# Kernel optimization log

Hardware: AMD Instinct MI355X
Metric: run time of the kernel (lower is better)

Reference implementation:

```python
import jax, jax.numpy as jnp
import numpy as np

DIM = 1024
N_HEADS = 16
HEAD_DIM = DIM // N_HEADS
FREQS = [31.0, 37.0, 41.0, 43.0, 47.0]
TWO_PI = 2.0 * float(np.pi)


def setup_inputs() -> dict:
    key = jax.random.key(0)
    ks = jax.random.split(key, 16)
    B, L = 2, 1024
    s = 0.02
    inp = {
        'x': jax.random.normal(ks[0], (B, L, DIM), dtype=jnp.float32),
        'Wq': jax.random.normal(ks[1], (DIM, DIM), dtype=jnp.float32) * s,
        'bq': jnp.zeros((DIM,), dtype=jnp.float32),
        'Wk': jax.random.normal(ks[2], (DIM, DIM), dtype=jnp.float32) * s,
        'bk': jnp.zeros((DIM,), dtype=jnp.float32),
        'Wv': jax.random.normal(ks[3], (DIM, DIM), dtype=jnp.float32) * s,
        'bv': jnp.zeros((DIM,), dtype=jnp.float32),
        'Wo': jax.random.normal(ks[4], (DIM, DIM), dtype=jnp.float32) * s,
        'bo': jnp.zeros((DIM,), dtype=jnp.float32),
        'alpha': jax.random.normal(ks[5], (N_HEADS, len(FREQS)), dtype=jnp.float32) * 0.1,
        'phi': jax.random.uniform(ks[6], (N_HEADS, len(FREQS)), dtype=jnp.float32) * TWO_PI,
        'temperature': jnp.ones((1,), dtype=jnp.float32),
        'gamma': jnp.ones((DIM,), dtype=jnp.float32),
        'beta': jnp.zeros((DIM,), dtype=jnp.float32),
    }
    return inp


def reference(x, Wq, bq, Wk, bk, Wv, bv, Wo, bo, alpha, phi, temperature, gamma, beta):
    B, L, D = x.shape
    H, hd = N_HEADS, HEAD_DIM
    # projections (torch Linear: y = x @ W.T + b), split heads -> (B,H,L,hd)
    q = (x @ Wq.T + bq).reshape(B, L, H, hd).transpose(0, 2, 1, 3)
    k = (x @ Wk.T + bk).reshape(B, L, H, hd).transpose(0, 2, 1, 3)
    v = (x @ Wv.T + bv).reshape(B, L, H, hd).transpose(0, 2, 1, 3)
    # similarity (B,H,L,L)
    sim = jnp.einsum('bhid,bhjd->bhij', q, k) / jnp.sqrt(jnp.asarray(hd, x.dtype))
    temp = jnp.abs(temperature)[0] + 0.1
    sim = sim / temp
    # multi-frequency holographic scores: sum_f alpha_f * sin(2*pi*sim/p_f + phi_f)
    scores = jnp.zeros_like(sim)
    for fi, freq in enumerate(FREQS):
        a = alpha[:, fi][None, :, None, None]
        p = phi[:, fi][None, :, None, None]
        scores = scores + a * jnp.sin(TWO_PI * sim / freq + p)
    # sigmoid-sum normalization (not softmax)
    w = jax.nn.sigmoid(scores)
    w = w / (jnp.sum(w, axis=-1, keepdims=True) + 1e-10)
    out = jnp.einsum('bhij,bhjd->bhid', w, v)
    out = out.transpose(0, 2, 1, 3).reshape(B, L, D)
    out = out @ Wo.T + bo
    # LayerNorm (eps=1e-5, biased variance)
    mu = jnp.mean(out, axis=-1, keepdims=True)
    var = jnp.mean(jnp.square(out - mu), axis=-1, keepdims=True)
    return (out - mu) / jnp.sqrt(var + 1e-5) * gamma + beta
```

## Files before the change

kernel.cpp:

```cpp
#include <hip/hip_runtime.h>
#include <hip/hip_bf16.h>

typedef short bf16x8 __attribute__((ext_vector_type(8)));
typedef float f32x4 __attribute__((ext_vector_type(4)));

#define MFMA16(a, b, c) __builtin_amdgcn_mfma_f32_16x16x32_bf16(a, b, c, 0, 0, 0)

static constexpr int SEQ = 1024;
static constexpr int DIM = 1024;
static constexpr int NH = 16;
static constexpr int HD = 64;

#if __has_builtin(__builtin_amdgcn_rcpf)
#define FAST_RCP(x) __builtin_amdgcn_rcpf(x)
#else
#define FAST_RCP(x) (1.0f / (x))
#endif

#if __has_builtin(__builtin_amdgcn_exp2f)
#define EXP2F(x) __builtin_amdgcn_exp2f(x)
#else
#define EXP2F(x) exp2f(x)
#endif

__device__ __forceinline__ int swz(int r) { return r ^ (r >> 3); }

__device__ __forceinline__ void gload16(const __hip_bfloat16* g, __hip_bfloat16* l)
{
    typedef const __attribute__((address_space(1))) unsigned GU;
    typedef __attribute__((address_space(3))) unsigned LU;
    __builtin_amdgcn_global_load_lds((GU*)g, (LU*)l, 16, 0, 0);
}

__global__ __launch_bounds__(256) void cvt_all(
    const float* __restrict__ x,  const float* __restrict__ wq,
    const float* __restrict__ wk, const float* __restrict__ wv,
    const float* __restrict__ wo,
    __hip_bfloat16* __restrict__ xb,  __hip_bfloat16* __restrict__ wqb,
    __hip_bfloat16* __restrict__ wkb, __hip_bfloat16* __restrict__ wvb,
    __hip_bfloat16* __restrict__ wob)
{
    const int reg = blockIdx.y;
    const float* src; __hip_bfloat16* dst; int n;
    if      (reg == 0) { src = x;  dst = xb;  n = 2 * SEQ * DIM; }
    else if (reg == 1) { src = wq; dst = wqb; n = DIM * DIM; }
    else if (reg == 2) { src = wk; dst = wkb; n = DIM * DIM; }
    else if (reg == 3) { src = wv; dst = wvb; n = DIM * DIM; }
    else               { src = wo; dst = wob; n = DIM * DIM; }
    const int i = (blockIdx.x * 256 + threadIdx.x) * 4;
    if (i < n) {
        float4 v = *(const float4*)(src + i);
        __hip_bfloat16 t[4];
        t[0] = __float2bfloat16(v.x); t[1] = __float2bfloat16(v.y);
        t[2] = __float2bfloat16(v.z); t[3] = __float2bfloat16(v.w);
        *(ushort4*)(dst + i) = *(ushort4*)t;
    }
}

__global__ __launch_bounds__(256) void gemm_qkv(
    const __hip_bfloat16* __restrict__ A,
    const __hip_bfloat16* __restrict__ W0, const __hip_bfloat16* __restrict__ W1,
    const __hip_bfloat16* __restrict__ W2,
    const float* __restrict__ b0, const float* __restrict__ b1,
    const float* __restrict__ b2,
    __hip_bfloat16* __restrict__ Y0, __hip_bfloat16* __restrict__ Y1,
    __hip_bfloat16* __restrict__ Y2,
    int M, int N, int K)
{
    __shared__ __align__(16) __hip_bfloat16 As[64 * 64];
    __shared__ __align__(16) __hip_bfloat16 Ws[128 * 64];

    const int z = blockIdx.z;
    const __hip_bfloat16* W = (z == 0) ? W0 : ((z == 1) ? W1 : W2);
    const float* bias = (z == 0) ? b0 : ((z == 1) ? b1 : b2);
    __hip_bfloat16* Y = (z == 0) ? Y0 : ((z == 1) ? Y1 : Y2);

    const int tid = threadIdx.x;
    const int wv = tid >> 6, lane = tid & 63;
    const int col16 = lane & 15, quad = lane >> 4;
    const int m0 = blockIdx.x * 64, n0 = blockIdx.y * 128;
    const int wr = wv >> 1, wc = wv & 1;

    const int scol = ((tid & 7) ^ ((tid >> 3) & 7)) * 8;
    const __hip_bfloat16* ga = A + (size_t)(m0 + (tid >> 3)) * K + scol;
    const __hip_bfloat16* gb = W + (size_t)(n0 + (tid >> 3)) * K + scol;
    __hip_bfloat16* lA = As + wv * 512;
    __hip_bfloat16* lB = Ws + wv * 512;

    const int c7 = col16 & 7;
    const int so0 = ((quad)     ^ c7) * 8;
    const int so1 = ((quad + 4) ^ c7) * 8;
    const __hip_bfloat16* ar = As + (wr * 32 + col16) * 64;
    const __hip_bfloat16* br = Ws + (wc * 64 + col16) * 64;

    f32x4 acc[8] = {};

    for (int k0 = 0; k0 < K; k0 += 64) {
        gload16(ga + k0,                  lA);
        gload16(ga + k0 + (size_t)32 * K, lA + 2048);
        gload16(gb + k0,                  lB);
        gload16(gb + k0 + (size_t)32 * K, lB + 2048);
        gload16(gb + k0 + (size_t)64 * K, lB + 4096);
        gload16(gb + k0 + (size_t)96 * K, lB + 6144);
        __syncthreads();
#pragma unroll
        for (int kh = 0; kh < 2; ++kh) {
            const int so = (kh == 0) ? so0 : so1;
            bf16x8 af[2], bfm[4];
#pragma unroll
            for (int mt = 0; mt < 2; ++mt) af[mt] = *(const bf16x8*)(ar + mt * 16 * 64 + so);
#pragma unroll
            for (int nt = 0; nt < 4; ++nt) bfm[nt] = *(const bf16x8*)(br + nt * 16 * 64 + so);
#pragma unroll
            for (int mt = 0; mt < 2; ++mt)
#pragma unroll
                for (int nt = 0; nt < 4; ++nt)
                    acc[mt * 4 + nt] = MFMA16(af[mt], bfm[nt], acc[mt * 4 + nt]);
        }
        __syncthreads();
    }

#pragma unroll
    for (int nt = 0; nt < 4; ++nt) {
        const int n = n0 + wc * 64 + nt * 16 + col16;
        const float bv = bias[n];
#pragma unroll
        for (int mt = 0; mt < 2; ++mt) {
#pragma unroll
            for (int r = 0; r < 4; ++r) {
                const int m = m0 + wr * 32 + mt * 16 + quad * 4 + r;
                Y[(size_t)m * N + n] = __float2bfloat16(acc[mt * 4 + nt][r] + bv);
            }
        }
    }
}

__global__ __launch_bounds__(256) void gemm_osplit(
    const __hip_bfloat16* __restrict__ A,
    const __hip_bfloat16* __restrict__ W,
    const float* __restrict__ bias,
    float* __restrict__ Y0, float* __restrict__ Y1,
    int M, int N, int K)
{
    __shared__ __align__(16) __hip_bfloat16 As[64 * 64];
    __shared__ __align__(16) __hip_bfloat16 Ws[128 * 64];

    const int z = blockIdx.z;
    float* Y = (z == 0) ? Y0 : Y1;
    const int kb = z * 512;

    const int tid = threadIdx.x;
    const int wv = tid >> 6, lane = tid & 63;
    const int col16 = lane & 15, quad = lane >> 4;
    const int m0 = blockIdx.x * 64, n0 = blockIdx.y * 128;
    const int wr = wv >> 1, wc = wv & 1;

    const int scol = ((tid & 7) ^ ((tid >> 3) & 7)) * 8;
    const __hip_bfloat16* ga = A + (size_t)(m0 + (tid >> 3)) * K + scol + kb;
    const __hip_bfloat16* gb = W + (size_t)(n0 + (tid >> 3)) * K + scol + kb;
    __hip_bfloat16* lA = As + wv * 512;
    __hip_bfloat16* lB = Ws + wv * 512;

    const int c7 = col16 & 7;
    const int so0 = ((quad)     ^ c7) * 8;
    const int so1 = ((quad + 4) ^ c7) * 8;
    const __hip_bfloat16* ar = As + (wr * 32 + col16) * 64;
    const __hip_bfloat16* br = Ws + (wc * 64 + col16) * 64;

    f32x4 acc[8] = {};

    for (int k0 = 0; k0 < 512; k0 += 64) {
        gload16(ga + k0,                  lA);
        gload16(ga + k0 + (size_t)32 * K, lA + 2048);
        gload16(gb + k0,                  lB);
        gload16(gb + k0 + (size_t)32 * K, lB + 2048);
        gload16(gb + k0 + (size_t)64 * K, lB + 4096);
        gload16(gb + k0 + (size_t)96 * K, lB + 6144);
        __syncthreads();
#pragma unroll
        for (int kh = 0; kh < 2; ++kh) {
            const int so = (kh == 0) ? so0 : so1;
            bf16x8 af[2], bfm[4];
#pragma unroll
            for (int mt = 0; mt < 2; ++mt) af[mt] = *(const bf16x8*)(ar + mt * 16 * 64 + so);
#pragma unroll
            for (int nt = 0; nt < 4; ++nt) bfm[nt] = *(const bf16x8*)(br + nt * 16 * 64 + so);
#pragma unroll
            for (int mt = 0; mt < 2; ++mt)
#pragma unroll
                for (int nt = 0; nt < 4; ++nt)
                    acc[mt * 4 + nt] = MFMA16(af[mt], bfm[nt], acc[mt * 4 + nt]);
        }
        __syncthreads();
    }

#pragma unroll
    for (int nt = 0; nt < 4; ++nt) {
        const int n = n0 + wc * 64 + nt * 16 + col16;
        const float bv = (z == 0) ? bias[n] : 0.0f;
#pragma unroll
        for (int mt = 0; mt < 2; ++mt) {
#pragma unroll
            for (int r = 0; r < 4; ++r) {
                const int m = m0 + wr * 32 + mt * 16 + quad * 4 + r;
                Y[(size_t)m * N + n] = acc[mt * 4 + nt][r] + bv;
            }
        }
    }
}

__global__ __launch_bounds__(256) void attn_kernel(
    const __hip_bfloat16* __restrict__ Q,
    const __hip_bfloat16* __restrict__ K,
    const __hip_bfloat16* __restrict__ V,
    const float* __restrict__ alpha, const float* __restrict__ phi,
    const float* __restrict__ temperature,
    __hip_bfloat16* __restrict__ AO)
{
    __shared__ __align__(16) char smem[18432 + 5120];
    __hip_bfloat16* VtBase = (__hip_bfloat16*)smem;
    __hip_bfloat16* PlBase = (__hip_bfloat16*)(smem + 18432);
    float* Ocomb = (float*)smem;
    float* Dl    = (float*)(smem + 2 * 16 * 68 * 4);

    const int tid = threadIdx.x;
    const int wv = tid >> 6, lane = tid & 63;
    const int col16 = lane & 15, quad = lane >> 4;
    const int g = wv & 1, half = wv >> 1;

    const int bh = blockIdx.y, b = bh >> 4, h = bh & 15;
    const int i0 = blockIdx.x * 32 + g * 16;
    const size_t base = ((size_t)b * SEQ) * DIM + (size_t)h * HD;

    const float tempv = fabsf(temperature[0]) + 0.1f;
    const float simscale = 1.0f / (8.0f * tempv);
    const float freqs[5] = {31.0f, 37.0f, 41.0f, 43.0f, 47.0f};

    float p[8] = {0.f, 0.f, 0.f, 0.f, 0.f, 0.f, 0.f, 0.f};
#pragma unroll
    for (int f = 0; f < 5; ++f) {
        const float a  = alpha[h * 5 + f] * 1.44269504089f;
        const float ph = phi[h * 5 + f];
        const float sp = __sinf(ph), cp = __cosf(ph);
        const float c  = 6.28318530718f * simscale / freqs[f];
        const float c2 = c * c, c3 = c2 * c, c4 = c2 * c2;
        const float c5 = c4 * c, c6 = c4 * c2, c7 = c4 * c3;
        p[0] += a * sp;
        p[1] += a * cp * c;
        p[2] -= a * sp * c2 * 0.5f;
        p[3] -= a * cp * c3 * (1.0f / 6.0f);
        p[4] += a * sp * c4 * (1.0f / 24.0f);
        p[5] += a * cp * c5 * (1.0f / 120.0f);
        p[6] -= a * sp * c6 * (1.0f / 720.0f);
        p[7] -= a * cp * c7 * (1.0f / 5040.0f);
    }

    const __hip_bfloat16* qrow = Q + base + (size_t)(i0 + col16) * DIM + quad * 8;
    const bf16x8 qa0 = *(const bf16x8*)(qrow);
    const bf16x8 qa1 = *(const bf16x8*)(qrow + 32);

    const __hip_bfloat16* kbase = K + base + (size_t)col16 * DIM + quad * 8;

    const int tl = tid & 127;
    const int sc0 = (tl & 7) * 8;
    const int sx  = tl & 7;
    const int jj0 = (tl >> 3) * 2;
    __hip_bfloat16* VtH = VtBase + half * 64 * 72;
    __hip_bfloat16* rowp[8];
#pragma unroll
    for (int e = 0; e < 8; ++e) rowp[e] = VtH + (sc0 + (e ^ sx)) * 72;

    const __hip_bfloat16* vrd[4];
#pragma unroll
    for (int t = 0; t < 4; ++t)
        vrd[t] = VtH + swz(t * 16 + col16) * 72 + quad * 8;

    __hip_bfloat16* PlW = PlBase + wv * 16 * 40;
    const __hip_bfloat16* plr = PlW + swz(col16) * 40 + quad * 8;
    __hip_bfloat16* plw[4];
#pragma unroll
    for (int r = 0; r < 4; ++r) plw[r] = PlW + swz(quad * 4 + r) * 40;

    f32x4 o[4] = {};
    float denom[4] = {0.f, 0.f, 0.f, 0.f};

    bf16x8 vr[2][2];
    bf16x8 kf[4][2];

    {
        const int j0 = half * 512;
#pragma unroll
        for (int s = 0; s < 2; ++s) {
            const __hip_bfloat16* vp = V + base + (size_t)(j0 + jj0 + 32 * s) * DIM + sc0;
            vr[s][0] = *(const bf16x8*)(vp);
            vr[s][1] = *(const bf16x8*)(vp + DIM);
        }
#pragma unroll
        for (int u = 0; u < 4; ++u) {
            const __hip_bfloat16* kp = kbase + (size_t)(j0 + u * 16) * DIM;
            kf[u][0] = *(const bf16x8*)(kp);
            kf[u][1] = *(const bf16x8*)(kp + 32);
        }
    }

    for (int it = 0; it < 8; ++it) {
        __syncthreads();
#pragma unroll
        for (int s = 0; s < 2; ++s) {
#pragma unroll
            for (int e = 0; e < 8; ++e) {
                unsigned pk = ((unsigned)(unsigned short)vr[s][0][e]) |
                              (((unsigned)(unsigned short)vr[s][1][e]) << 16);
                *(unsigned*)(rowp[e] + jj0 + 32 * s) = pk;
            }
        }
        __syncthreads();

        const int j1 = half * 512 + (it + 1) * 64;
        if (it < 7) {
#pragma unroll
            for (int s = 0; s < 2; ++s) {
                const __hip_bfloat16* vp = V + base + (size_t)(j1 + jj0 + 32 * s) * DIM + sc0;
                vr[s][0] = *(const bf16x8*)(vp);
                vr[s][1] = *(const bf16x8*)(vp + DIM);
            }
        }

        f32x4 sa4[4];
#pragma unroll
        for (int u = 0; u < 4; ++u) {
            f32x4 zz = {};
            zz = MFMA16(qa0, kf[u][0], zz);
            zz = MFMA16(qa1, kf[u][1], zz);
            sa4[u] = zz;
        }

        if (it < 7) {
#pragma unroll
            for (int u = 0; u < 4; ++u) {
                const __hip_bfloat16* kp = kbase + (size_t)(j1 + u * 16) * DIM;
                kf[u][0] = *(const bf16x8*)(kp);
                kf[u][1] = *(const bf16x8*)(kp + 32);
            }
        }

#pragma unroll
        for (int sub = 0; sub < 2; ++sub) {
#pragma unroll
            for (int s2 = 0; s2 < 2; ++s2) {
                const int u = sub * 2 + s2;
#pragma unroll
                for (int r = 0; r < 4; ++r) {
                    const float sv = sa4[u][r];
                    float sc = fmaf(sv, p[7], p[6]);
                    sc = fmaf(sv, sc, p[5]);
                    sc = fmaf(sv, sc, p[4]);
                    sc = fmaf(sv, sc, p[3]);
                    sc = fmaf(sv, sc, p[2]);
                    sc = fmaf(sv, sc, p[1]);
                    sc = fmaf(sv, sc, p[0]);
                    const float w = FAST_RCP(1.0f + EXP2F(-sc));
                    denom[r] += w;
                    plw[r][s2 * 16 + col16] = __float2bfloat16(w);
                }
            }
            bf16x8 pa = *(const bf16x8*)plr;
#pragma unroll
            for (int t = 0; t < 4; ++t) {
                bf16x8 vb = *(const bf16x8*)(vrd[t] + 32 * sub);
                o[t] = MFMA16(pa, vb, o[t]);
            }
        }
    }

#pragma unroll
    for (int r = 0; r < 4; ++r) {
        float d = denom[r];
        d += __shfl_xor(d, 1);
        d += __shfl_xor(d, 2);
        d += __shfl_xor(d, 4);
        d += __shfl_xor(d, 8);
        denom[r] = d;
    }

    __syncthreads();
    if (half == 1) {
#pragma unroll
        for (int t = 0; t < 4; ++t)
#pragma unroll
            for (int r = 0; r < 4; ++r)
                Ocomb[(g * 16 + quad * 4 + r) * 68 + t * 16 + col16] = o[t][r];
        if (col16 == 0) {
#pragma unroll
            for (int r = 0; r < 4; ++r) Dl[g * 16 + quad * 4 + r] = denom[r];
        }
    }
    __syncthreads();
    if (half == 0) {
#pragma unroll
        for (int r = 0; r < 4; ++r)
            denom[r] = denom[r] + Dl[g * 16 + quad * 4 + r] + 1e-10f;
#pragma unroll
        for (int t = 0; t < 4; ++t) {
#pragma unroll
            for (int r = 0; r < 4; ++r) {
                const float val =
                    (o[t][r] + Ocomb[(g * 16 + quad * 4 + r) * 68 + t * 16 + col16]) / denom[r];
                const size_t row = (size_t)b * SEQ + i0 + quad * 4 + r;
                AO[row * DIM + h * HD + t * 16 + col16] = __float2bfloat16(val);
            }
        }
    }
}

__global__ __launch_bounds__(256) void ln_kernel(
    const float* __restrict__ Yp0,
    const float* __restrict__ Yp1,
    const float* __restrict__ gamma,
    const float* __restrict__ beta,
    float* __restrict__ out)
{
    const int row = blockIdx.x;
    const float* y0 = Yp0 + (size_t)row * DIM;
    const float* y1 = Yp1 + (size_t)row * DIM;

    float v[4];
    float s = 0.f, s2 = 0.f;
#pragma unroll
    for (int e = 0; e < 4; ++e) {
        const int idx = threadIdx.x + e * 256;
        v[e] = y0[idx] + y1[idx];
        s += v[e];
        s2 += v[e] * v[e];
    }
#pragma unroll
    for (int off = 1; off < 64; off <<= 1) {
        s  += __shfl_xor(s, off);
        s2 += __shfl_xor(s2, off);
    }
    __shared__ float ps[4], ps2[4];
    const int wave = threadIdx.x >> 6;
    if ((threadIdx.x & 63) == 0) { ps[wave] = s; ps2[wave] = s2; }
    __syncthreads();
    s  = ps[0] + ps[1] + ps[2] + ps[3];
    s2 = ps2[0] + ps2[1] + ps2[2] + ps2[3];

    const float mu   = s * (1.0f / DIM);
    const float var  = s2 * (1.0f / DIM) - mu * mu;
    const float rstd = rsqrtf(var + 1e-5f);

#pragma unroll
    for (int e = 0; e < 4; ++e) {
        const int idx = threadIdx.x + e * 256;
        out[(size_t)row * DIM + idx] =
            (v[e] - mu) * rstd * gamma[idx] + beta[idx];
    }
}

extern "C" void kernel_launch(void* const* d_in, const int* in_sizes, int n_in,
                              void* d_out, int out_size, void* d_ws, size_t ws_size,
                              hipStream_t stream)
{
    const float* x     = (const float*)d_in[0];
    const float* Wq    = (const float*)d_in[1];
    const float* bq    = (const float*)d_in[2];
    const float* Wk    = (const float*)d_in[3];
    const float* bk    = (const float*)d_in[4];
    const float* Wv    = (const float*)d_in[5];
    const float* bv    = (const float*)d_in[6];
    const float* Wo    = (const float*)d_in[7];
    const float* bo    = (const float*)d_in[8];
    const float* alpha = (const float*)d_in[9];
    const float* phi   = (const float*)d_in[10];
    const float* temp  = (const float*)d_in[11];
    const float* gamma = (const float*)d_in[12];
    const float* beta  = (const float*)d_in[13];

    float* out = (float*)d_out;

    const int B = 2;
    const int M = B * SEQ;

    char* wsb = (char*)d_ws;
    __hip_bfloat16* xb  = (__hip_bfloat16*)(wsb + 0);
    __hip_bfloat16* Wqb = (__hip_bfloat16*)(wsb + (4u  << 20));
    __hip_bfloat16* Wkb = (__hip_bfloat16*)(wsb + (6u  << 20));
    __hip_bfloat16* Wvb = (__hip_bfloat16*)(wsb + (8u  << 20));
    __hip_bfloat16* Wob = (__hip_bfloat16*)(wsb + (10u << 20));
    __hip_bfloat16* Qb  = (__hip_bfloat16*)(wsb + (12u << 20));
    __hip_bfloat16* Kb  = (__hip_bfloat16*)(wsb + (16u << 20));
    __hip_bfloat16* Vb  = (__hip_bfloat16*)(wsb + (20u << 20));
    __hip_bfloat16* AO  = (__hip_bfloat16*)(wsb + (24u << 20));
    float*          Yp0 = (float*)(wsb + 0);
    float*          Yp1 = (float*)(wsb + (12u << 20));

    hipLaunchKernelGGL(cvt_all, dim3(2048, 5), dim3(256), 0, stream,
                       x, Wq, Wk, Wv, Wo, xb, Wqb, Wkb, Wvb, Wob);

    hipLaunchKernelGGL(gemm_qkv, dim3(M / 64, DIM / 128, 3), dim3(256), 0, stream,
                       xb, Wqb, Wkb, Wvb, bq, bk, bv, Qb, Kb, Vb, M, DIM, DIM);

    hipLaunchKernelGGL(attn_kernel, dim3(SEQ / 32, B * NH), dim3(256), 0, stream,
                       Qb, Kb, Vb, alpha, phi, temp, AO);

    hipLaunchKernelGGL(gemm_osplit, dim3(M / 64, DIM / 128, 2), dim3(256), 0, stream,
                       AO, Wob, bo, Yp0, Yp1, M, DIM, DIM);

    hipLaunchKernelGGL(ln_kernel, dim3(M), dim3(256), 0, stream,
                       Yp0, Yp1, gamma, beta, out);
}
```

Before: 171.2 us.

## Keep attention weights in registers via transposed QK MFMA and lane shuffles

The QK^T MFMA operands are swapped so each lane holds score columns rather than rows. The sigmoid weights can then be packed to bf16 in registers and exchanged across lanes with shuffles to form the PV A-operand, instead of a round trip through an LDS staging buffer. The V transpose store permutes its key columns to match the new register ordering, and the denominator reduction is simplified to match the new layout. It also adds s_setprio around the MFMA blocks, trading LDS traffic for cross-lane shuffles and more complex index mapping.

New measurement: 169.6 us. Within noise of the previous version (-0.9%).

```diff
diff --git a/kernel.cpp b/kernel.cpp
--- a/kernel.cpp
+++ b/kernel.cpp
@@ -30,6 +30,13 @@
     typedef const __attribute__((address_space(1))) unsigned GU;
     typedef __attribute__((address_space(3))) unsigned LU;
     __builtin_amdgcn_global_load_lds((GU*)g, (LU*)l, 16, 0, 0);
+}
+
+__device__ __forceinline__ unsigned pack2bf(float a, float b)
+{
+    union { __hip_bfloat16 h; unsigned short u; } ca, cb;
+    ca.h = __float2bfloat16(a); cb.h = __float2bfloat16(b);
+    return (unsigned)ca.u | ((unsigned)cb.u << 16);
 }
 
 __global__ __launch_bounds__(256) void cvt_all(
@@ -217,9 +224,8 @@
     const float* __restrict__ temperature,
     __hip_bfloat16* __restrict__ AO)
 {
-    __shared__ __align__(16) char smem[18432 + 5120];
+    __shared__ __align__(16) char smem[18432 + 512];
     __hip_bfloat16* VtBase = (__hip_bfloat16*)smem;
-    __hip_bfloat16* PlBase = (__hip_bfloat16*)(smem + 18432);
     float* Ocomb = (float*)smem;
     float* Dl    = (float*)(smem + 2 * 16 * 68 * 4);
 
@@ -265,6 +271,8 @@
     const int sc0 = (tl & 7) * 8;
     const int sx  = tl & 7;
     const int jj0 = (tl >> 3) * 2;
+    const int pu = (jj0 >> 4) & 1, pqs = (jj0 >> 2) & 3, pr = jj0 & 3;
+    const int col0 = ((pqs ^ (pu << 1)) << 3) + (pu << 2) + pr;
     __hip_bfloat16* VtH = VtBase + half * 64 * 72;
     __hip_bfloat16* rowp[8];
 #pragma unroll
@@ -275,14 +283,8 @@
     for (int t = 0; t < 4; ++t)
         vrd[t] = VtH + swz(t * 16 + col16) * 72 + quad * 8;
 
-    __hip_bfloat16* PlW = PlBase + wv * 16 * 40;
-    const __hip_bfloat16* plr = PlW + swz(col16) * 40 + quad * 8;
-    __hip_bfloat16* plw[4];
-#pragma unroll
-    for (int r = 0; r < 4; ++r) plw[r] = PlW + swz(quad * 4 + r) * 40;
-
     f32x4 o[4] = {};
-    float denom[4] = {0.f, 0.f, 0.f, 0.f};
+    float denomL = 0.f;
 
     bf16x8 vr[2][2];
     bf16x8 kf[4][2];
@@ -311,7 +313,7 @@
             for (int e = 0; e < 8; ++e) {
                 unsigned pk = ((unsigned)(unsigned short)vr[s][0][e]) |
                               (((unsigned)(unsigned short)vr[s][1][e]) << 16);
-                *(unsigned*)(rowp[e] + jj0 + 32 * s) = pk;
+                *(unsigned*)(rowp[e] + col0 + 32 * s) = pk;
             }
         }
         __syncthreads();
@@ -327,13 +329,15 @@
         }
 
         f32x4 sa4[4];
+        __builtin_amdgcn_s_setprio(1);
 #pragma unroll
         for (int u = 0; u < 4; ++u) {
             f32x4 zz = {};
-            zz = MFMA16(qa0, kf[u][0], zz);
-            zz = MFMA16(qa1, kf[u][1], zz);
+            zz = MFMA16(kf[u][0], qa0, zz);
+            zz = MFMA16(kf[u][1], qa1, zz);
             sa4[u] = zz;
         }
+        __builtin_amdgcn_s_setprio(0);
 
         if (it < 7) {
 #pragma unroll
@@ -346,6 +350,7 @@
 
 #pragma unroll
         for (int sub = 0; sub < 2; ++sub) {
+            float w[2][4];
 #pragma unroll
             for (int s2 = 0; s2 < 2; ++s2) {
                 const int u = sub * 2 + s2;
@@ -359,53 +364,55 @@
                     sc = fmaf(sv, sc, p[2]);
                     sc = fmaf(sv, sc, p[1]);
                     sc = fmaf(sv, sc, p[0]);
-                    const float w = FAST_RCP(1.0f + EXP2F(-sc));
-                    denom[r] += w;
-                    plw[r][s2 * 16 + col16] = __float2bfloat16(w);
+                    const float ww = FAST_RCP(1.0f + EXP2F(-sc));
+                    denomL += ww;
+                    w[s2][r] = ww;
                 }
             }
-            bf16x8 pa = *(const bf16x8*)plr;
+            const unsigned pk00 = pack2bf(w[0][0], w[0][1]);
+            const unsigned pk01 = pack2bf(w[0][2], w[0][3]);
+            const unsigned pk10 = pack2bf(w[1][0], w[1][1]);
+            const unsigned pk11 = pack2bf(w[1][2], w[1][3]);
+            const unsigned sw0 = (unsigned)__shfl_xor((int)pk10, 32);
+            const unsigned sw1 = (unsigned)__shfl_xor((int)pk11, 32);
+            union { unsigned d[4]; bf16x8 v; } pu8;
+            pu8.d[0] = pk00; pu8.d[1] = pk01; pu8.d[2] = sw0; pu8.d[3] = sw1;
+            const bf16x8 pa = pu8.v;
+
+            __builtin_amdgcn_s_setprio(1);
 #pragma unroll
             for (int t = 0; t < 4; ++t) {
                 bf16x8 vb = *(const bf16x8*)(vrd[t] + 32 * sub);
                 o[t] = MFMA16(pa, vb, o[t]);
             }
-        }
-    }
-
-#pragma unroll
-    for (int r = 0; r < 4; ++r) {
-        float d = denom[r];
-        d += __shfl_xor(d, 1);
-        d += __shfl_xor(d, 2);
-        d += __shfl_xor(d, 4);
-        d += __shfl_xor(d, 8);
-        denom[r] = d;
-    }
+            __builtin_amdgcn_s_setprio(0);
+        }
+    }
+
+    denomL += __shfl_xor(denomL, 16);
+    denomL += __shfl_xor(denomL, 32);
 
     __syncthreads();
+    if (quad == 0) Dl[half * 32 + g * 16 + col16] = denomL;
     if (half == 1) {
 #pragma unroll
         for (int t = 0; t < 4; ++t)
 #pragma unroll
             for (int r = 0; r < 4; ++r)
                 Ocomb[(g * 16 + quad * 4 + r) * 68 + t * 16 + col16] = o[t][r];
-        if (col16 == 0) {
-#pragma unroll
-            for (int r = 0; r < 4; ++r) Dl[g * 16 + quad * 4 + r] = denom[r];
-        }
     }
     __syncthreads();
     if (half == 0) {
+        float dn[4];
 #pragma unroll
         for (int r = 0; r < 4; ++r)
-            denom[r] = denom[r] + Dl[g * 16 + quad * 4 + r] + 1e-10f;
+            dn[r] = Dl[g * 16 + quad * 4 + r] + Dl[32 + g * 16 + quad * 4 + r] + 1e-10f;
 #pragma unroll
         for (int t = 0; t < 4; ++t) {
 #pragma unroll
             for (int r = 0; r < 4; ++r) {
                 const float val =
-                    (o[t][r] + Ocomb[(g * 16 + quad * 4 + r) * 68 + t * 16 + col16]) / denom[r];
+                    (o[t][r] + Ocomb[(g * 16 + quad * 4 + r) * 68 + t * 16 + col16]) / dn[r];
                 const size_t row = (size_t)b * SEQ + i0 + quad * 4 + r;
                 AO[row * DIM + h * HD + t * 16 + col16] = __float2bfloat16(val);
             }
```
